# Kernel optimization log

Measured on AMD Instinct MI355X. Metric: run time of the kernel, lower is better.

The kernel has to match this reference:

```python
import jax, jax.numpy as jnp
import numpy as np

B, L, D, K, V = 256, 50, 128, 4, 50000
LENGTH = 5      # opt.length
BETA = 0.01     # opt.beta scaling on loss1
EPS = 1e-12     # F.normalize eps


def _l2norm(x, axis):
    n = jnp.sqrt(jnp.sum(x * x, axis=axis, keepdims=True))
    return x / jnp.maximum(n, EPS)


def setup_inputs() -> dict:
    key = jax.random.key(0)
    ks = jax.random.split(key, 11)
    s = 1.0 / np.sqrt(D)  # reset_parameters: uniform(-stdv, stdv)
    u = lambda k, shape: jax.random.uniform(k, shape, jnp.float32, -s, s)
    return {
        "hidden": jax.random.normal(ks[0], (B, L, D), jnp.float32),
        "mask": jnp.ones((B, L), jnp.int32),
        "pos_emb": u(ks[1], (L, D)),
        "w1": u(ks[2], (2 * D, D)),
        "w2": u(ks[3], (D, K)),
        "glu1_w": u(ks[4], (D, K * D)),
        "glu1_b": u(ks[5], (K * D,)),
        "att_w1": u(ks[6], (D, D)),
        "att_w2": u(ks[7], (D, D)),
        "att_v": u(ks[8], (D, K)),
        "emb": u(ks[9], (V, D)),
    }


def reference(hidden, mask, pos_emb, w1, w2, glu1_w, glu1_b, att_w1, att_w2, att_v, emb):
    m = mask.astype(jnp.float32)[..., None]                       # [B,L,1]
    hs = jnp.sum(hidden * m, axis=1) / jnp.sum(m, axis=1)         # [B,D] masked mean
    # nh = tanh(cat(pos, hidden) @ w1); then sigmoid(glu1)
    cat = jnp.concatenate([jnp.broadcast_to(pos_emb[None], hidden.shape), hidden], axis=-1)
    nh = jnp.tanh(cat @ w1)                                       # [B,L,D]
    nh = jax.nn.sigmoid(nh @ glu1_w + glu1_b)                     # [B,L,K*D]
    # torch.split(dim=2) + stack(dim=3) -> [B,L,D,K]
    nh = nh.reshape(B, L, K, D).transpose(0, 1, 3, 2)             # [B,L,D,K]
    beta = jnp.einsum('bldk,dk->blk', nh, w2)                     # [B,L,K]
    # attention gate alpha = sigmoid(att_v(tanh(W1 hs + W2 hidden)))
    att = jnp.tanh(hs[:, None, :] @ att_w1 + hidden @ att_w2)     # [B,L,D]
    alpha = jax.nn.sigmoid(att @ att_v)                           # [B,L,K]
    beta = beta * (0.5 + alpha) * m                               # mask over interests
    # per-interest L2 normalize along sequence (fused over K)
    nb = _l2norm(beta, axis=1)                                    # [B,L,K]
    # pairwise |cos| between interests: vectorized Gram instead of python loops
    G = jnp.einsum('bli,blj->bij', nb, nb)                        # [B,K,K]
    triu = jnp.triu(jnp.ones((K, K), jnp.float32), 1)
    sim = jnp.sum(jnp.abs(G) * triu, axis=(1, 2)) * (2.0 / (K * (K - 1)))  # [B]
    lens = jnp.sum(mask, axis=1).astype(jnp.float32) - LENGTH     # sumask[:,0] - length
    loss1 = jnp.sum(jax.nn.sigmoid(sim * lens))                   # scalar
    # per-interest pooled session reps, stacked on leading axis -> [K,B,D]
    select = jnp.einsum('blk,bld->kbd', beta, hidden)
    b_norm = _l2norm(emb[1:], axis=-1)                            # [V-1,D]
    scores = jnp.einsum('kbd,vd->kbv', select, b_norm)            # [K,B,V-1]
    max_scores = jnp.max(scores, axis=0)                          # [B,V-1]
    return (max_scores, loss1 * BETA, scores)
```

## Files before the change

### kernel.cpp

```cpp
#include <hip/hip_runtime.h>
#include <hip/hip_bf16.h>
#include <math.h>

constexpr int NB = 256;
constexpr int NL = 50;
constexpr int ND = 128;
constexpr int NK = 4;
constexpr int NVm1 = 49999;
constexpr int NPAD2 = 50176;
constexpr int ROWS = NB * NL;
constexpr int MROWS = NB * NK;
constexpr int GEMM_NT = 4;

typedef __bf16 bf16x8 __attribute__((ext_vector_type(8)));
typedef float f32x4 __attribute__((ext_vector_type(4)));

__device__ __forceinline__ float sigm_fast(float x) { return 1.0f / (1.0f + __expf(-x)); }
__device__ __forceinline__ float sigm_prec(float x) { return 1.0f / (1.0f + expf(-x)); }

__device__ __forceinline__ void gld_lds16(const void* g, void* l) {
    __builtin_amdgcn_global_load_lds(
        (const __attribute__((address_space(1))) void*)g,
        (__attribute__((address_space(3))) void*)l, 16, 0, 0);
}

__global__ void k_hs(const float* __restrict__ hidden, const int* __restrict__ mask,
                     float* __restrict__ hs, float* __restrict__ loss_out) {
    int b = blockIdx.x;
    int d = threadIdx.x;
    float acc = 0.f, msum = 0.f;
    for (int l = 0; l < NL; ++l) {
        float mv = (float)mask[b * NL + l];
        acc += hidden[((size_t)b * NL + l) * ND + d] * mv;
        msum += mv;
    }
    hs[b * ND + d] = acc / msum;
    if (b == 0 && d == 0) loss_out[0] = 0.f;
}

__global__ void k_rowmats(const float* __restrict__ pos_emb, const float* __restrict__ w1,
                          const float* __restrict__ hs, const float* __restrict__ att_w1,
                          float* __restrict__ posPart, float* __restrict__ hsW1) {
    int r = blockIdx.x;
    int d = threadIdx.x;
    const float *src, *mat;
    float* dst;
    if (r < NL) { src = pos_emb + (size_t)r * ND; mat = w1;     dst = posPart + (size_t)r * ND; }
    else        { int b = r - NL; src = hs + (size_t)b * ND; mat = att_w1; dst = hsW1 + (size_t)b * ND; }
    __shared__ float s[ND];
    s[d] = src[d];
    __syncthreads();
    float acc = 0.f;
#pragma unroll 8
    for (int j = 0; j < ND; ++j) acc += s[j] * mat[j * ND + d];
    dst[d] = acc;
}

__global__ __launch_bounds__(256) void k_nh_att(
    const float* __restrict__ hidden, const float* __restrict__ w1,
    const float* __restrict__ att_w2, const float* __restrict__ att_v,
    const float* __restrict__ posPart, const float* __restrict__ hsW1,
    float* __restrict__ nh_out, float* __restrict__ alpha_out) {
    constexpr int R = 32;
    __shared__ float X[R * ND];
    __shared__ float ATT[R * 132];
    int row0 = blockIdx.x * R;
    int tid = threadIdx.x;
    for (int i = tid; i < R * ND; i += 256) X[i] = hidden[(size_t)row0 * ND + i];
    __syncthreads();
    int d = tid & 127;
    int rg = tid >> 7;
    float accN[16], accA[16];
#pragma unroll
    for (int r = 0; r < 16; ++r) { accN[r] = 0.f; accA[r] = 0.f; }
    const float4* Xv = (const float4*)X;
    for (int j4 = 0; j4 < 32; ++j4) {
        float w1v[4], awv[4];
#pragma unroll
        for (int u = 0; u < 4; ++u) {
            int j = j4 * 4 + u;
            w1v[u] = w1[(ND + j) * ND + d];
            awv[u] = att_w2[j * ND + d];
        }
#pragma unroll
        for (int r = 0; r < 16; ++r) {
            float4 xv = Xv[(rg * 16 + r) * 32 + j4];
            accN[r] = fmaf(xv.w, w1v[3], fmaf(xv.z, w1v[2], fmaf(xv.y, w1v[1], fmaf(xv.x, w1v[0], accN[r]))));
            accA[r] = fmaf(xv.w, awv[3], fmaf(xv.z, awv[2], fmaf(xv.y, awv[1], fmaf(xv.x, awv[0], accA[r]))));
        }
    }
#pragma unroll
    for (int r = 0; r < 16; ++r) {
        int row = row0 + rg * 16 + r;
        int b = row / NL;
        int l = row - b * NL;
        float nhv = tanhf(posPart[l * ND + d] + accN[r]);
        float atv = tanhf(hsW1[b * ND + d] + accA[r]);
        nh_out[(size_t)row * ND + d] = nhv;
        ATT[(rg * 16 + r) * 132 + d] = atv;
    }
    __syncthreads();
    if (tid < 128) {
        int rl = tid >> 2;
        int k = tid & 3;
        float acc = 0.f;
        for (int dd = 0; dd < ND; ++dd) acc += ATT[rl * 132 + dd] * att_v[dd * NK + k];
        alpha_out[(size_t)(row0 + rl) * NK + k] = sigm_fast(acc);
    }
}

__global__ __launch_bounds__(256) void k_glu_beta(
    const float* __restrict__ nh, const float* __restrict__ glu1_w,
    const float* __restrict__ glu1_b, const float* __restrict__ w2,
    const float* __restrict__ alpha, const int* __restrict__ mask,
    float* __restrict__ beta_out) {
    constexpr int R = 16;
    __shared__ float NHs[R * ND];
    __shared__ float P[R * 513];
    int row0 = blockIdx.x * R;
    int tid = threadIdx.x;
    for (int i = tid; i < R * ND; i += 256) NHs[i] = nh[(size_t)row0 * ND + i];
    __syncthreads();
    float acc0[R], acc1[R];
#pragma unroll
    for (int r = 0; r < R; ++r) { acc0[r] = 0.f; acc1[r] = 0.f; }
    int c0 = tid, c1 = tid + 256;
    const float4* Nv = (const float4*)NHs;
    for (int j4 = 0; j4 < 32; ++j4) {
        float g0v[4], g1v[4];
#pragma unroll
        for (int u = 0; u < 4; ++u) {
            int j = j4 * 4 + u;
            g0v[u] = glu1_w[j * 512 + c0];
            g1v[u] = glu1_w[j * 512 + c1];
        }
#pragma unroll
        for (int r = 0; r < R; ++r) {
            float4 xv = Nv[r * 32 + j4];
            acc0[r] = fmaf(xv.w, g0v[3], fmaf(xv.z, g0v[2], fmaf(xv.y, g0v[1], fmaf(xv.x, g0v[0], acc0[r]))));
            acc1[r] = fmaf(xv.w, g1v[3], fmaf(xv.z, g1v[2], fmaf(xv.y, g1v[1], fmaf(xv.x, g1v[0], acc1[r]))));
        }
    }
    float bb0 = glu1_b[c0], bb1 = glu1_b[c1];
    float w20 = w2[(c0 & 127) * NK + (c0 >> 7)];
    float w21 = w2[(c1 & 127) * NK + (c1 >> 7)];
#pragma unroll
    for (int r = 0; r < R; ++r) {
        P[r * 513 + c0] = sigm_fast(acc0[r] + bb0) * w20;
        P[r * 513 + c1] = sigm_fast(acc1[r] + bb1) * w21;
    }
    __syncthreads();
    if (tid < 64) {
        int r = tid >> 2;
        int k = tid & 3;
        float s = 0.f;
        for (int dd = 0; dd < ND; ++dd) s += P[r * 513 + k * ND + dd];
        int row = row0 + r;
        float mv = (float)mask[row];
        float a = alpha[(size_t)row * NK + k];
        beta_out[(size_t)row * NK + k] = s * (0.5f + a) * mv;
    }
}

__global__ void k_loss(const float* __restrict__ beta, const int* __restrict__ mask,
                       float* __restrict__ loss_out) {
    int b = blockIdx.x;
    int t = threadIdx.x;
    float mv = (t < NL) ? (float)mask[b * NL + t] : 0.f;
    float msum = mv;
    for (int off = 32; off >= 1; off >>= 1) msum += __shfl_xor(msum, off);
    float lens = msum - 5.0f;
    float bk[NK] = {0.f, 0.f, 0.f, 0.f};
    if (t < NL) {
#pragma unroll
        for (int k = 0; k < NK; ++k) bk[k] = beta[((size_t)b * NL + t) * NK + k];
    }
    float nb[NK];
#pragma unroll
    for (int k = 0; k < NK; ++k) {
        float v = bk[k] * bk[k];
        for (int off = 32; off >= 1; off >>= 1) v += __shfl_xor(v, off);
        nb[k] = bk[k] / fmaxf(sqrtf(v), 1e-12f);
    }
    float sim = 0.f;
#pragma unroll
    for (int i = 0; i < NK; ++i) {
#pragma unroll
        for (int j = 0; j < NK; ++j) {
            if (j > i) {
                float p = nb[i] * nb[j];
                for (int off = 32; off >= 1; off >>= 1) p += __shfl_xor(p, off);
                sim += fabsf(p);
            }
        }
    }
    sim *= (2.0f / (NK * (NK - 1)));
    if (t == 0) atomicAdd(loss_out, sigm_prec(sim * lens) * 0.01f);
}

__global__ __launch_bounds__(256) void k_sel_bnorm(
    const float* __restrict__ beta, const float* __restrict__ hidden,
    const float* __restrict__ emb, __hip_bfloat16* __restrict__ selb,
    __hip_bfloat16* __restrict__ bnv) {
    int blk = blockIdx.x;
    int tid = threadIdx.x;
    if (blk < NPAD2 / 2) {
        int v = blk * 2 + (tid >> 7);
        int j = tid & 127;
        __shared__ float red[4];
        float x = 0.f;
        if (v < NVm1) x = emb[((size_t)v + 1) * ND + j];
        float ss = x * x;
        for (int off = 32; off >= 1; off >>= 1) ss += __shfl_xor(ss, off);
        int w = tid >> 6;
        if ((tid & 63) == 0) red[w] = ss;
        __syncthreads();
        float tot = (tid < 128) ? (red[0] + red[1]) : (red[2] + red[3]);
        float rn = 1.f / fmaxf(sqrtf(tot), 1e-12f);
        bnv[(size_t)v * ND + j] = __float2bfloat16(x * rn);
    } else {
        int b = (blk - NPAD2 / 2) * 2 + (tid >> 7);
        int d = tid & 127;
        float a0 = 0.f, a1 = 0.f, a2 = 0.f, a3 = 0.f;
        for (int l = 0; l < NL; ++l) {
            float h = hidden[((size_t)b * NL + l) * ND + d];
            const float* bp = &beta[((size_t)b * NL + l) * NK];
            a0 = fmaf(bp[0], h, a0);
            a1 = fmaf(bp[1], h, a1);
            a2 = fmaf(bp[2], h, a2);
            a3 = fmaf(bp[3], h, a3);
        }
        selb[((size_t)b * NK + 0) * ND + d] = __float2bfloat16(a0);
        selb[((size_t)b * NK + 1) * ND + d] = __float2bfloat16(a1);
        selb[((size_t)b * NK + 2) * ND + d] = __float2bfloat16(a2);
        selb[((size_t)b * NK + 3) * ND + d] = __float2bfloat16(a3);
    }
}

__global__ __launch_bounds__(256) void k_gemm(
    const __hip_bfloat16* __restrict__ selb, const __hip_bfloat16* __restrict__ bn,
    float* __restrict__ scores, float* __restrict__ maxs) {
    __shared__ __hip_bfloat16 As[128 * 128];
    __shared__ __hip_bfloat16 Bs[128 * 128];
    int bm0 = blockIdx.y * 128;
    int nbase = blockIdx.x * (128 * GEMM_NT);
    int tid = threadIdx.x;
    int wave = tid >> 6, lane = tid & 63;
    int l16 = lane & 15, quad = lane >> 4;
    int m_loc = (wave >> 1) * 64;
    int n_loc = (wave & 1) * 64;

#pragma unroll
    for (int it = 0; it < 8; ++it) {
        int id = it * 256 + tid;
        int row = id >> 4, c = id & 15;
        int gc = c ^ (row & 7);
        const char* g = (const char*)selb + ((size_t)(bm0 + row) * 16 + gc) * 16;
        char* l = (char*)As + (size_t)(it * 256 + wave * 64) * 16;
        gld_lds16(g, l);
    }

    const bf16x8* Av = (const bf16x8*)As;
    const bf16x8* Bv = (const bf16x8*)Bs;

    for (int nt = 0; nt < GEMM_NT; ++nt) {
        int bn0 = nbase + nt * 128;
#pragma unroll
        for (int it = 0; it < 8; ++it) {
            int id = it * 256 + tid;
            int row = id >> 4, c = id & 15;
            int gc = c ^ (row & 7);
            const char* g = (const char*)bn + ((size_t)(bn0 + row) * 16 + gc) * 16;
            char* l = (char*)Bs + (size_t)(it * 256 + wave * 64) * 16;
            gld_lds16(g, l);
        }
        __syncthreads();

        f32x4 acc[4][4];
#pragma unroll
        for (int mi = 0; mi < 4; ++mi)
#pragma unroll
            for (int ni = 0; ni < 4; ++ni) acc[mi][ni] = (f32x4){0.f, 0.f, 0.f, 0.f};

#pragma unroll
        for (int kk = 0; kk < 4; ++kk) {
            int ko = kk * 4 + quad;
            bf16x8 afr[4], bfr[4];
#pragma unroll
            for (int mi = 0; mi < 4; ++mi) {
                int row = m_loc + mi * 16 + l16;
                afr[mi] = Av[row * 16 + (ko ^ (row & 7))];
            }
#pragma unroll
            for (int ni = 0; ni < 4; ++ni) {
                int row = n_loc + ni * 16 + l16;
                bfr[ni] = Bv[row * 16 + (ko ^ (row & 7))];
            }
#pragma unroll
            for (int mi = 0; mi < 4; ++mi)
#pragma unroll
                for (int ni = 0; ni < 4; ++ni)
                    acc[mi][ni] = __builtin_amdgcn_mfma_f32_16x16x32_bf16(
                        afr[mi], bfr[ni], acc[mi][ni], 0, 0, 0);
        }

#pragma unroll
        for (int mi = 0; mi < 4; ++mi) {
            int m_base = bm0 + m_loc + mi * 16;
            int bidx = (m_base >> 2) + quad;
#pragma unroll
            for (int ni = 0; ni < 4; ++ni) {
                int n = bn0 + n_loc + ni * 16 + l16;
                if (n < NVm1) {
                    float mx = acc[mi][ni][0];
#pragma unroll
                    for (int r = 0; r < 4; ++r) {
                        float val = acc[mi][ni][r];
                        scores[(size_t)r * NB * NVm1 + (size_t)bidx * NVm1 + n] = val;
                        mx = fmaxf(mx, val);
                    }
                    maxs[(size_t)bidx * NVm1 + n] = mx;
                }
            }
        }
        __syncthreads();
    }
}

extern "C" void kernel_launch(void* const* d_in, const int* in_sizes, int n_in,
                              void* d_out, int out_size, void* d_ws, size_t ws_size,
                              hipStream_t stream) {
    const float* hidden  = (const float*)d_in[0];
    const int*   mask    = (const int*)d_in[1];
    const float* pos_emb = (const float*)d_in[2];
    const float* w1      = (const float*)d_in[3];
    const float* w2      = (const float*)d_in[4];
    const float* glu1_w  = (const float*)d_in[5];
    const float* glu1_b  = (const float*)d_in[6];
    const float* att_w1  = (const float*)d_in[7];
    const float* att_w2  = (const float*)d_in[8];
    const float* att_v   = (const float*)d_in[9];
    const float* emb     = (const float*)d_in[10];

    float* out      = (float*)d_out;
    float* max_out  = out;
    float* loss_out = out + (size_t)NB * NVm1;
    float* scores   = out + (size_t)NB * NVm1 + 1;

    char* w = (char*)d_ws;
    auto alloc = [&](size_t bytes) {
        char* p = w;
        w += (bytes + 255) & ~(size_t)255;
        return p;
    };
    float* posPart = (float*)alloc((size_t)NL * ND * 4);
    float* hs      = (float*)alloc((size_t)NB * ND * 4);
    float* hsW1    = (float*)alloc((size_t)NB * ND * 4);
    float* nh      = (float*)alloc((size_t)ROWS * ND * 4);
    float* alphav  = (float*)alloc((size_t)ROWS * NK * 4);
    float* betav   = (float*)alloc((size_t)ROWS * NK * 4);
    __hip_bfloat16* selb = (__hip_bfloat16*)alloc((size_t)MROWS * ND * 2);
    __hip_bfloat16* bnv  = (__hip_bfloat16*)alloc((size_t)NPAD2 * ND * 2);

    k_hs<<<NB, 128, 0, stream>>>(hidden, mask, hs, loss_out);
    k_rowmats<<<NL + NB, 128, 0, stream>>>(pos_emb, w1, hs, att_w1, posPart, hsW1);
    k_nh_att<<<ROWS / 32, 256, 0, stream>>>(hidden, w1, att_w2, att_v, posPart, hsW1, nh, alphav);
    k_glu_beta<<<ROWS / 16, 256, 0, stream>>>(nh, glu1_w, glu1_b, w2, alphav, mask, betav);
    k_loss<<<NB, 64, 0, stream>>>(betav, mask, loss_out);
    k_sel_bnorm<<<NPAD2 / 2 + NB / 2, 256, 0, stream>>>(betav, hidden, emb, selb, bnv);
    k_gemm<<<dim3(NPAD2 / (128 * GEMM_NT), MROWS / 128), 256, 0, stream>>>(selb, bnv, scores, max_out);
}
```

Baseline: 488.3 us.

## Fuse nh/attention/GLU stages into one bf16 MFMA kernel with prep pass

Replaces the fp32 FMA kernels for nh, the attention gate and the GLU/beta stage with one fused kernel. It converts hidden and the transposed weights to bf16 and runs all three matmuls on MFMA, keeping nh and alpha in LDS so they are not written to global memory. A prep kernel merges the hs, posPart, embedding normalisation and bf16 conversions into one launch, and a fast exp-based tanh replaces tanhf. The intent is to cut FP32 ALU time, global traffic and launch count, at the cost of bf16 precision in the intermediate activations.

```diff
diff --git a/kernel.cpp b/kernel.cpp
--- a/kernel.cpp
+++ b/kernel.cpp
@@ -11,12 +11,27 @@
 constexpr int ROWS = NB * NL;
 constexpr int MROWS = NB * NK;
 constexpr int GEMM_NT = 4;
+constexpr int MR = 64;
+
+constexpr int G_BN  = NPAD2 / 2;
+constexpr int G_HS  = NB / 2;
+constexpr int G_PP  = NL / 2;
+constexpr int G_XB  = ROWS * ND / 2048;
+constexpr int G_W1T = ND * ND / 256;
+constexpr int G_AWT = ND * ND / 256;
+constexpr int G_GLT = ND * 512 / 256;
+constexpr int G_TOT = G_BN + G_HS + G_PP + G_XB + G_W1T + G_AWT + G_GLT;
 
 typedef __bf16 bf16x8 __attribute__((ext_vector_type(8)));
 typedef float f32x4 __attribute__((ext_vector_type(4)));
 
 __device__ __forceinline__ float sigm_fast(float x) { return 1.0f / (1.0f + __expf(-x)); }
 __device__ __forceinline__ float sigm_prec(float x) { return 1.0f / (1.0f + expf(-x)); }
+__device__ __forceinline__ float fast_tanh(float x) {
+    float xc = fminf(fmaxf(x, -15.f), 15.f);
+    float e = __expf(2.f * xc);
+    return (e - 1.f) / (e + 1.f);
+}
 
 __device__ __forceinline__ void gld_lds16(const void* g, void* l) {
     __builtin_amdgcn_global_load_lds(
@@ -24,141 +39,237 @@
         (__attribute__((address_space(3))) void*)l, 16, 0, 0);
 }
 
-__global__ void k_hs(const float* __restrict__ hidden, const int* __restrict__ mask,
-                     float* __restrict__ hs, float* __restrict__ loss_out) {
-    int b = blockIdx.x;
-    int d = threadIdx.x;
-    float acc = 0.f, msum = 0.f;
-    for (int l = 0; l < NL; ++l) {
-        float mv = (float)mask[b * NL + l];
-        acc += hidden[((size_t)b * NL + l) * ND + d] * mv;
-        msum += mv;
-    }
-    hs[b * ND + d] = acc / msum;
-    if (b == 0 && d == 0) loss_out[0] = 0.f;
-}
-
-__global__ void k_rowmats(const float* __restrict__ pos_emb, const float* __restrict__ w1,
-                          const float* __restrict__ hs, const float* __restrict__ att_w1,
-                          float* __restrict__ posPart, float* __restrict__ hsW1) {
-    int r = blockIdx.x;
-    int d = threadIdx.x;
-    const float *src, *mat;
-    float* dst;
-    if (r < NL) { src = pos_emb + (size_t)r * ND; mat = w1;     dst = posPart + (size_t)r * ND; }
-    else        { int b = r - NL; src = hs + (size_t)b * ND; mat = att_w1; dst = hsW1 + (size_t)b * ND; }
-    __shared__ float s[ND];
-    s[d] = src[d];
+__global__ __launch_bounds__(256) void k_prep(
+    const float* __restrict__ hidden, const int* __restrict__ mask,
+    const float* __restrict__ pos_emb, const float* __restrict__ w1,
+    const float* __restrict__ att_w2, const float* __restrict__ glu1_w,
+    const float* __restrict__ emb,
+    float* __restrict__ hs, float* __restrict__ posPart,
+    __hip_bfloat16* __restrict__ XbG, __hip_bfloat16* __restrict__ w1h_t,
+    __hip_bfloat16* __restrict__ attw2_t, __hip_bfloat16* __restrict__ glu_t,
+    __hip_bfloat16* __restrict__ bnv, float* __restrict__ loss_out) {
+    __shared__ float sPP[2 * ND];
+    __shared__ float red[4];
+    int blk = blockIdx.x, tid = threadIdx.x;
+    if (blk < G_BN) {
+        int v = blk * 2 + (tid >> 7);
+        int j = tid & 127;
+        float x = 0.f;
+        if (v < NVm1) x = emb[((size_t)v + 1) * ND + j];
+        float ss = x * x;
+        for (int off = 32; off >= 1; off >>= 1) ss += __shfl_xor(ss, off);
+        if ((tid & 63) == 0) red[tid >> 6] = ss;
+        __syncthreads();
+        float tot = (tid < 128) ? (red[0] + red[1]) : (red[2] + red[3]);
+        float rn = 1.f / fmaxf(sqrtf(tot), 1e-12f);
+        bnv[(size_t)v * ND + j] = __float2bfloat16(x * rn);
+    } else if (blk < G_BN + G_HS) {
+        int b = (blk - G_BN) * 2 + (tid >> 7);
+        int d = tid & 127;
+        float acc = 0.f, msum = 0.f;
+        for (int l = 0; l < NL; ++l) {
+            float mv = (float)mask[b * NL + l];
+            acc += hidden[((size_t)b * NL + l) * ND + d] * mv;
+            msum += mv;
+        }
+        hs[b * ND + d] = acc / msum;
+        if (blk == G_BN && tid == 0) loss_out[0] = 0.f;
+    } else if (blk < G_BN + G_HS + G_PP) {
+        int rel = blk - (G_BN + G_HS);
+        int rl = tid >> 7, d = tid & 127;
+        int r = rel * 2 + rl;
+        sPP[rl * ND + d] = pos_emb[r * ND + d];
+        __syncthreads();
+        float acc = 0.f;
+#pragma unroll 8
+        for (int j = 0; j < ND; ++j) acc += sPP[rl * ND + j] * w1[j * ND + d];
+        posPart[r * ND + d] = acc;
+    } else if (blk < G_BN + G_HS + G_PP + G_XB) {
+        int rel = blk - (G_BN + G_HS + G_PP);
+        size_t base = (size_t)rel * 2048 + (size_t)tid * 8;
+        float4 f0 = *(const float4*)&hidden[base];
+        float4 f1 = *(const float4*)&hidden[base + 4];
+        union { bf16x8 v; __hip_bfloat16 h[8]; } u;
+        u.h[0] = __float2bfloat16(f0.x); u.h[1] = __float2bfloat16(f0.y);
+        u.h[2] = __float2bfloat16(f0.z); u.h[3] = __float2bfloat16(f0.w);
+        u.h[4] = __float2bfloat16(f1.x); u.h[5] = __float2bfloat16(f1.y);
+        u.h[6] = __float2bfloat16(f1.z); u.h[7] = __float2bfloat16(f1.w);
+        *(bf16x8*)&XbG[base] = u.v;
+    } else if (blk < G_BN + G_HS + G_PP + G_XB + G_W1T) {
+        int i = (blk - (G_BN + G_HS + G_PP + G_XB)) * 256 + tid;
+        int d = i >> 7, j = i & 127;
+        w1h_t[d * ND + j] = __float2bfloat16(w1[(ND + j) * ND + d]);
+    } else if (blk < G_BN + G_HS + G_PP + G_XB + G_W1T + G_AWT) {
+        int i = (blk - (G_BN + G_HS + G_PP + G_XB + G_W1T)) * 256 + tid;
+        int d = i >> 7, j = i & 127;
+        attw2_t[d * ND + j] = __float2bfloat16(att_w2[j * ND + d]);
+    } else {
+        int i = (blk - (G_BN + G_HS + G_PP + G_XB + G_W1T + G_AWT)) * 256 + tid;
+        int c = i >> 7, j = i & 127;
+        glu_t[c * ND + j] = __float2bfloat16(glu1_w[j * 512 + c]);
+    }
+}
+
+__global__ __launch_bounds__(256) void k_mega(
+    const __hip_bfloat16* __restrict__ XbG, const __hip_bfloat16* __restrict__ w1h_t,
+    const __hip_bfloat16* __restrict__ attw2_t, const __hip_bfloat16* __restrict__ glu_t,
+    const float* __restrict__ hs, const float* __restrict__ att_w1,
+    const float* __restrict__ att_v, const float* __restrict__ posPart,
+    const float* __restrict__ glu1_b, const float* __restrict__ w2,
+    const int* __restrict__ mask, float* __restrict__ beta_out) {
+    __shared__ __hip_bfloat16 XbS[MR * ND];
+    __shared__ __hip_bfloat16 WS[ND * ND];
+    __shared__ __attribute__((aligned(16))) __hip_bfloat16 NHS[MR * 136];
+    __shared__ float alphaS[MR * NK];
+    __shared__ float hsW1S[3 * ND];
+    int row0 = blockIdx.x * MR;
+    int tid = threadIdx.x;
+    int wave = tid >> 6, lane = tid & 63, l16 = lane & 15, quad = lane >> 4;
+    int b0 = row0 / NL;
+
+#pragma unroll
+    for (int it = 0; it < 4; ++it) {
+        int id = it * 256 + tid;
+        int row = id >> 4, c = id & 15, gc = c ^ (row & 7);
+        gld_lds16((const char*)XbG + ((size_t)(row0 + row) * 16 + gc) * 16,
+                  (char*)XbS + (size_t)(it * 256 + wave * 64) * 16);
+    }
+#pragma unroll
+    for (int it = 0; it < 8; ++it) {
+        int id = it * 256 + tid;
+        int row = id >> 4, c = id & 15, gc = c ^ (row & 7);
+        gld_lds16((const char*)attw2_t + ((size_t)row * 16 + gc) * 16,
+                  (char*)WS + (size_t)(it * 256 + wave * 64) * 16);
+    }
+    for (int i = tid; i < 3 * ND; i += 256) {
+        int bb = i >> 7, d = i & 127, b = b0 + bb;
+        float acc = 0.f;
+        if (b < NB) {
+            for (int j = 0; j < ND; ++j) acc += hs[b * ND + j] * att_w1[j * ND + d];
+        }
+        hsW1S[i] = acc;
+    }
     __syncthreads();
-    float acc = 0.f;
-#pragma unroll 8
-    for (int j = 0; j < ND; ++j) acc += s[j] * mat[j * ND + d];
-    dst[d] = acc;
-}
-
-__global__ __launch_bounds__(256) void k_nh_att(
-    const float* __restrict__ hidden, const float* __restrict__ w1,
-    const float* __restrict__ att_w2, const float* __restrict__ att_v,
-    const float* __restrict__ posPart, const float* __restrict__ hsW1,
-    float* __restrict__ nh_out, float* __restrict__ alpha_out) {
-    constexpr int R = 32;
-    __shared__ float X[R * ND];
-    __shared__ float ATT[R * 132];
-    int row0 = blockIdx.x * R;
-    int tid = threadIdx.x;
-    for (int i = tid; i < R * ND; i += 256) X[i] = hidden[(size_t)row0 * ND + i];
+
+    const bf16x8* Xv = (const bf16x8*)XbS;
+    const bf16x8* Wv = (const bf16x8*)WS;
+    const bf16x8* Nv = (const bf16x8*)NHS;
+    int arow = wave * 16 + l16;
+
+    f32x4 acc8[8];
+#pragma unroll
+    for (int ni = 0; ni < 8; ++ni) acc8[ni] = (f32x4){0.f, 0.f, 0.f, 0.f};
+#pragma unroll
+    for (int kk = 0; kk < 4; ++kk) {
+        int ko = kk * 4 + quad;
+        bf16x8 af = Xv[arow * 16 + (ko ^ (arow & 7))];
+#pragma unroll
+        for (int ni = 0; ni < 8; ++ni) {
+            int n = ni * 16 + l16;
+            bf16x8 bf = Wv[n * 16 + (ko ^ (n & 7))];
+            acc8[ni] = __builtin_amdgcn_mfma_f32_16x16x32_bf16(af, bf, acc8[ni], 0, 0, 0);
+        }
+    }
+#pragma unroll
+    for (int r = 0; r < 4; ++r) {
+        int lrow = wave * 16 + quad * 4 + r;
+        int grow = row0 + lrow;
+        int bb = grow / NL - b0;
+        float a0 = 0.f, a1 = 0.f, a2 = 0.f, a3 = 0.f;
+#pragma unroll
+        for (int ni = 0; ni < 8; ++ni) {
+            int col = ni * 16 + l16;
+            float atv = fast_tanh(hsW1S[bb * ND + col] + acc8[ni][r]);
+            float4 av = *(const float4*)&att_v[col * 4];
+            a0 += atv * av.x; a1 += atv * av.y; a2 += atv * av.z; a3 += atv * av.w;
+        }
+#pragma unroll
+        for (int off = 1; off < 16; off <<= 1) {
+            a0 += __shfl_xor(a0, off); a1 += __shfl_xor(a1, off);
+            a2 += __shfl_xor(a2, off); a3 += __shfl_xor(a3, off);
+        }
+        if (l16 == 0) {
+            alphaS[lrow * 4 + 0] = sigm_fast(a0);
+            alphaS[lrow * 4 + 1] = sigm_fast(a1);
+            alphaS[lrow * 4 + 2] = sigm_fast(a2);
+            alphaS[lrow * 4 + 3] = sigm_fast(a3);
+        }
+    }
     __syncthreads();
-    int d = tid & 127;
-    int rg = tid >> 7;
-    float accN[16], accA[16];
-#pragma unroll
-    for (int r = 0; r < 16; ++r) { accN[r] = 0.f; accA[r] = 0.f; }
-    const float4* Xv = (const float4*)X;
-    for (int j4 = 0; j4 < 32; ++j4) {
-        float w1v[4], awv[4];
-#pragma unroll
-        for (int u = 0; u < 4; ++u) {
-            int j = j4 * 4 + u;
-            w1v[u] = w1[(ND + j) * ND + d];
-            awv[u] = att_w2[j * ND + d];
-        }
-#pragma unroll
-        for (int r = 0; r < 16; ++r) {
-            float4 xv = Xv[(rg * 16 + r) * 32 + j4];
-            accN[r] = fmaf(xv.w, w1v[3], fmaf(xv.z, w1v[2], fmaf(xv.y, w1v[1], fmaf(xv.x, w1v[0], accN[r]))));
-            accA[r] = fmaf(xv.w, awv[3], fmaf(xv.z, awv[2], fmaf(xv.y, awv[1], fmaf(xv.x, awv[0], accA[r]))));
-        }
-    }
-#pragma unroll
-    for (int r = 0; r < 16; ++r) {
-        int row = row0 + rg * 16 + r;
-        int b = row / NL;
-        int l = row - b * NL;
-        float nhv = tanhf(posPart[l * ND + d] + accN[r]);
-        float atv = tanhf(hsW1[b * ND + d] + accA[r]);
-        nh_out[(size_t)row * ND + d] = nhv;
-        ATT[(rg * 16 + r) * 132 + d] = atv;
+#pragma unroll
+    for (int it = 0; it < 8; ++it) {
+        int id = it * 256 + tid;
+        int row = id >> 4, c = id & 15, gc = c ^ (row & 7);
+        gld_lds16((const char*)w1h_t + ((size_t)row * 16 + gc) * 16,
+                  (char*)WS + (size_t)(it * 256 + wave * 64) * 16);
     }
     __syncthreads();
-    if (tid < 128) {
-        int rl = tid >> 2;
-        int k = tid & 3;
-        float acc = 0.f;
-        for (int dd = 0; dd < ND; ++dd) acc += ATT[rl * 132 + dd] * att_v[dd * NK + k];
-        alpha_out[(size_t)(row0 + rl) * NK + k] = sigm_fast(acc);
-    }
-}
-
-__global__ __launch_bounds__(256) void k_glu_beta(
-    const float* __restrict__ nh, const float* __restrict__ glu1_w,
-    const float* __restrict__ glu1_b, const float* __restrict__ w2,
-    const float* __restrict__ alpha, const int* __restrict__ mask,
-    float* __restrict__ beta_out) {
-    constexpr int R = 16;
-    __shared__ float NHs[R * ND];
-    __shared__ float P[R * 513];
-    int row0 = blockIdx.x * R;
-    int tid = threadIdx.x;
-    for (int i = tid; i < R * ND; i += 256) NHs[i] = nh[(size_t)row0 * ND + i];
+#pragma unroll
+    for (int ni = 0; ni < 8; ++ni) acc8[ni] = (f32x4){0.f, 0.f, 0.f, 0.f};
+#pragma unroll
+    for (int kk = 0; kk < 4; ++kk) {
+        int ko = kk * 4 + quad;
+        bf16x8 af = Xv[arow * 16 + (ko ^ (arow & 7))];
+#pragma unroll
+        for (int ni = 0; ni < 8; ++ni) {
+            int n = ni * 16 + l16;
+            bf16x8 bf = Wv[n * 16 + (ko ^ (n & 7))];
+            acc8[ni] = __builtin_amdgcn_mfma_f32_16x16x32_bf16(af, bf, acc8[ni], 0, 0, 0);
+        }
+    }
+#pragma unroll
+    for (int r = 0; r < 4; ++r) {
+        int lrow = wave * 16 + quad * 4 + r;
+        int grow = row0 + lrow;
+        int l = grow % NL;
+#pragma unroll
+        for (int ni = 0; ni < 8; ++ni) {
+            int col = ni * 16 + l16;
+            float nhv = fast_tanh(posPart[l * ND + col] + acc8[ni][r]);
+            NHS[lrow * 136 + col] = __float2bfloat16(nhv);
+        }
+    }
     __syncthreads();
-    float acc0[R], acc1[R];
-#pragma unroll
-    for (int r = 0; r < R; ++r) { acc0[r] = 0.f; acc1[r] = 0.f; }
-    int c0 = tid, c1 = tid + 256;
-    const float4* Nv = (const float4*)NHs;
-    for (int j4 = 0; j4 < 32; ++j4) {
-        float g0v[4], g1v[4];
-#pragma unroll
-        for (int u = 0; u < 4; ++u) {
-            int j = j4 * 4 + u;
-            g0v[u] = glu1_w[j * 512 + c0];
-            g1v[u] = glu1_w[j * 512 + c1];
-        }
-#pragma unroll
-        for (int r = 0; r < R; ++r) {
-            float4 xv = Nv[r * 32 + j4];
-            acc0[r] = fmaf(xv.w, g0v[3], fmaf(xv.z, g0v[2], fmaf(xv.y, g0v[1], fmaf(xv.x, g0v[0], acc0[r]))));
-            acc1[r] = fmaf(xv.w, g1v[3], fmaf(xv.z, g1v[2], fmaf(xv.y, g1v[1], fmaf(xv.x, g1v[0], acc1[r]))));
-        }
-    }
-    float bb0 = glu1_b[c0], bb1 = glu1_b[c1];
-    float w20 = w2[(c0 & 127) * NK + (c0 >> 7)];
-    float w21 = w2[(c1 & 127) * NK + (c1 >> 7)];
-#pragma unroll
-    for (int r = 0; r < R; ++r) {
-        P[r * 513 + c0] = sigm_fast(acc0[r] + bb0) * w20;
-        P[r * 513 + c1] = sigm_fast(acc1[r] + bb1) * w21;
-    }
-    __syncthreads();
-    if (tid < 64) {
-        int r = tid >> 2;
-        int k = tid & 3;
-        float s = 0.f;
-        for (int dd = 0; dd < ND; ++dd) s += P[r * 513 + k * ND + dd];
-        int row = row0 + r;
-        float mv = (float)mask[row];
-        float a = alpha[(size_t)row * NK + k];
-        beta_out[(size_t)row * NK + k] = s * (0.5f + a) * mv;
+    for (int ch = 0; ch < 4; ++ch) {
+#pragma unroll
+        for (int it = 0; it < 8; ++it) {
+            int id = it * 256 + tid;
+            int row = id >> 4, c = id & 15, gc = c ^ (row & 7);
+            gld_lds16((const char*)glu_t + ((size_t)(ch * ND + row) * 16 + gc) * 16,
+                      (char*)WS + (size_t)(it * 256 + wave * 64) * 16);
+        }
+        __syncthreads();
+#pragma unroll
+        for (int ni = 0; ni < 8; ++ni) acc8[ni] = (f32x4){0.f, 0.f, 0.f, 0.f};
+#pragma unroll
+        for (int kk = 0; kk < 4; ++kk) {
+            int ko = kk * 4 + quad;
+            bf16x8 af = Nv[arow * 17 + ko];
+#pragma unroll
+            for (int ni = 0; ni < 8; ++ni) {
+                int n = ni * 16 + l16;
+                bf16x8 bf = Wv[n * 16 + (ko ^ (n & 7))];
+                acc8[ni] = __builtin_amdgcn_mfma_f32_16x16x32_bf16(af, bf, acc8[ni], 0, 0, 0);
+            }
+        }
+#pragma unroll
+        for (int r = 0; r < 4; ++r) {
+            float s = 0.f;
+#pragma unroll
+            for (int ni = 0; ni < 8; ++ni) {
+                int col = ni * 16 + l16;
+                s += sigm_fast(acc8[ni][r] + glu1_b[ch * ND + col]) * w2[col * 4 + ch];
+            }
+#pragma unroll
+            for (int off = 1; off < 16; off <<= 1) s += __shfl_xor(s, off);
+            if (l16 == 0) {
+                int lrow = wave * 16 + quad * 4 + r;
+                int grow = row0 + lrow;
+                float a = alphaS[lrow * 4 + ch];
+                beta_out[(size_t)grow * 4 + ch] = s * (0.5f + a) * (float)mask[grow];
+            }
+        }
+        __syncthreads();
     }
 }
 
@@ -198,43 +309,24 @@
     if (t == 0) atomicAdd(loss_out, sigm_prec(sim * lens) * 0.01f);
 }
 
-__global__ __launch_bounds__(256) void k_sel_bnorm(
+__global__ __launch_bounds__(256) void k_select(
     const float* __restrict__ beta, const float* __restrict__ hidden,
-    const float* __restrict__ emb, __hip_bfloat16* __restrict__ selb,
-    __hip_bfloat16* __restrict__ bnv) {
-    int blk = blockIdx.x;
-    int tid = threadIdx.x;
-    if (blk < NPAD2 / 2) {
-        int v = blk * 2 + (tid >> 7);
-        int j = tid & 127;
-        __shared__ float red[4];
-        float x = 0.f;
-        if (v < NVm1) x = emb[((size_t)v + 1) * ND + j];
-        float ss = x * x;
-        for (int off = 32; off >= 1; off >>= 1) ss += __shfl_xor(ss, off);
-        int w = tid >> 6;
-        if ((tid & 63) == 0) red[w] = ss;
-        __syncthreads();
-        float tot = (tid < 128) ? (red[0] + red[1]) : (red[2] + red[3]);
-        float rn = 1.f / fmaxf(sqrtf(tot), 1e-12f);
-        bnv[(size_t)v * ND + j] = __float2bfloat16(x * rn);
-    } else {
-        int b = (blk - NPAD2 / 2) * 2 + (tid >> 7);
-        int d = tid & 127;
-        float a0 = 0.f, a1 = 0.f, a2 = 0.f, a3 = 0.f;
-        for (int l = 0; l < NL; ++l) {
-            float h = hidden[((size_t)b * NL + l) * ND + d];
-            const float* bp = &beta[((size_t)b * NL + l) * NK];
-            a0 = fmaf(bp[0], h, a0);
-            a1 = fmaf(bp[1], h, a1);
-            a2 = fmaf(bp[2], h, a2);
-            a3 = fmaf(bp[3], h, a3);
-        }
-        selb[((size_t)b * NK + 0) * ND + d] = __float2bfloat16(a0);
-        selb[((size_t)b * NK + 1) * ND + d] = __float2bfloat16(a1);
-        selb[((size_t)b * NK + 2) * ND + d] = __float2bfloat16(a2);
-        selb[((size_t)b * NK + 3) * ND + d] = __float2bfloat16(a3);
-    }
+    __hip_bfloat16* __restrict__ selb) {
+    int b = blockIdx.x * 2 + (threadIdx.x >> 7);
+    int d = threadIdx.x & 127;
+    float a0 = 0.f, a1 = 0.f, a2 = 0.f, a3 = 0.f;
+    for (int l = 0; l < NL; ++l) {
+        float h = hidden[((size_t)b * NL + l) * ND + d];
+        const float* bp = &beta[((size_t)b * NL + l) * NK];
+        a0 = fmaf(bp[0], h, a0);
+        a1 = fmaf(bp[1], h, a1);
+        a2 = fmaf(bp[2], h, a2);
+        a3 = fmaf(bp[3], h, a3);
+    }
+    selb[((size_t)b * NK + 0) * ND + d] = __float2bfloat16(a0);
+    selb[((size_t)b * NK + 1) * ND + d] = __float2bfloat16(a1);
+    selb[((size_t)b * NK + 2) * ND + d] = __float2bfloat16(a2);
+    selb[((size_t)b * NK + 3) * ND + d] = __float2bfloat16(a3);
 }
 
 __global__ __launch_bounds__(256) void k_gemm(
@@ -253,11 +345,9 @@
 #pragma unroll
     for (int it = 0; it < 8; ++it) {
         int id = it * 256 + tid;
-        int row = id >> 4, c = id & 15;
-        int gc = c ^ (row & 7);
-        const char* g = (const char*)selb + ((size_t)(bm0 + row) * 16 + gc) * 16;
-        char* l = (char*)As + (size_t)(it * 256 + wave * 64) * 16;
-        gld_lds16(g, l);
+        int row = id >> 4, c = id & 15, gc = c ^ (row & 7);
+        gld_lds16((const char*)selb + ((size_t)(bm0 + row) * 16 + gc) * 16,
+                  (char*)As + (size_t)(it * 256 + wave * 64) * 16);
     }
 
     const bf16x8* Av = (const bf16x8*)As;
@@ -268,11 +358,9 @@
 #pragma unroll
         for (int it = 0; it < 8; ++it) {
             int id = it * 256 + tid;
-            int row = id >> 4, c = id & 15;
-            int gc = c ^ (row & 7);
-            const char* g = (const char*)bn + ((size_t)(bn0 + row) * 16 + gc) * 16;
-            char* l = (char*)Bs + (size_t)(it * 256 + wave * 64) * 16;
-            gld_lds16(g, l);
+            int row = id >> 4, c = id & 15, gc = c ^ (row & 7);
+            gld_lds16((const char*)bn + ((size_t)(bn0 + row) * 16 + gc) * 16,
+                      (char*)Bs + (size_t)(it * 256 + wave * 64) * 16);
         }
         __syncthreads();
 
@@ -355,18 +443,19 @@
     };
     float* posPart = (float*)alloc((size_t)NL * ND * 4);
     float* hs      = (float*)alloc((size_t)NB * ND * 4);
-    float* hsW1    = (float*)alloc((size_t)NB * ND * 4);
-    float* nh      = (float*)alloc((size_t)ROWS * ND * 4);
-    float* alphav  = (float*)alloc((size_t)ROWS * NK * 4);
     float* betav   = (float*)alloc((size_t)ROWS * NK * 4);
-    __hip_bfloat16* selb = (__hip_bfloat16*)alloc((size_t)MROWS * ND * 2);
-    __hip_bfloat16* bnv  = (__hip_bfloat16*)alloc((size_t)NPAD2 * ND * 2);
-
-    k_hs<<<NB, 128, 0, stream>>>(hidden, mask, hs, loss_out);
-    k_rowmats<<<NL + NB, 128, 0, stream>>>(pos_emb, w1, hs, att_w1, posPart, hsW1);
-    k_nh_att<<<ROWS / 32, 256, 0, stream>>>(hidden, w1, att_w2, att_v, posPart, hsW1, nh, alphav);
-    k_glu_beta<<<ROWS / 16, 256, 0, stream>>>(nh, glu1_w, glu1_b, w2, alphav, mask, betav);
+    __hip_bfloat16* XbG     = (__hip_bfloat16*)alloc((size_t)ROWS * ND * 2);
+    __hip_bfloat16* w1h_t   = (__hip_bfloat16*)alloc((size_t)ND * ND * 2);
+    __hip_bfloat16* attw2_t = (__hip_bfloat16*)alloc((size_t)ND * ND * 2);
+    __hip_bfloat16* glu_t   = (__hip_bfloat16*)alloc((size_t)512 * ND * 2);
+    __hip_bfloat16* selb    = (__hip_bfloat16*)alloc((size_t)MROWS * ND * 2);
+    __hip_bfloat16* bnv     = (__hip_bfloat16*)alloc((size_t)NPAD2 * ND * 2);
+
+    k_prep<<<G_TOT, 256, 0, stream>>>(hidden, mask, pos_emb, w1, att_w2, glu1_w, emb,
+                                      hs, posPart, XbG, w1h_t, attw2_t, glu_t, bnv, loss_out);
+    k_mega<<<ROWS / MR, 256, 0, stream>>>(XbG, w1h_t, attw2_t, glu_t, hs, att_w1,
+                                          att_v, posPart, glu1_b, w2, mask, betav);
     k_loss<<<NB, 64, 0, stream>>>(betav, mask, loss_out);
-    k_sel_bnorm<<<NPAD2 / 2 + NB / 2, 256, 0, stream>>>(betav, hidden, emb, selb, bnv);
+    k_select<<<NB / 2, 256, 0, stream>>>(betav, hidden, selb);
     k_gemm<<<dim3(NPAD2 / (128 * GEMM_NT), MROWS / 128), 256, 0, stream>>>(selb, bnv, scores, max_out);
 }
```

After: 435.3 us. -10.8%, faster.
